# Performance work log

Measured on AMD Instinct MI355X. Metric: run time of the kernel, lower is better.

Reference implementation:

```python
import jax, jax.numpy as jnp
import numpy as np
from jax import lax

CONF_THRES = 0.5
IOU_THRES = 0.45
TOP_K = 2048  # fixed candidate cap for jit-friendly NMS


def _xywh2xyxy(x):
    # x: [N,4] center-x, center-y, w, h -> x1,y1,x2,y2
    xy, wh = x[:, :2], x[:, 2:4]
    return jnp.concatenate([xy - wh / 2, xy + wh / 2], axis=-1)


def _box_iou(b1, b2):
    # b1: [N,4], b2: [M,4] in xyxy -> [N,M]
    area1 = (b1[:, 2] - b1[:, 0]) * (b1[:, 3] - b1[:, 1])
    area2 = (b2[:, 2] - b2[:, 0]) * (b2[:, 3] - b2[:, 1])
    lt = jnp.maximum(b1[:, None, :2], b2[None, :, :2])
    rb = jnp.minimum(b1[:, None, 2:], b2[None, :, 2:])
    inter = jnp.clip(rb - lt, 0).prod(-1)
    return inter / (area1[:, None] + area2[None, :] - inter)


def _nms_per_image(x):
    # x: [N,16] = xywh(4), obj(1), landmarks(10), cls_score(1); nc=1 path
    obj = x[:, 4]
    conf = x[:, 15] * obj          # x[:,15:] *= x[:,4:5], then max over 1 class
    box = _xywh2xyxy(x[:, :4])
    valid = (obj > CONF_THRES) & (conf > CONF_THRES)
    score = jnp.where(valid, conf, -jnp.inf)

    topv, topi = lax.top_k(score, TOP_K)          # sorted descending
    valid_k = jnp.isfinite(topv)                  # [K]
    boxes_k = box[topi]                           # [K,4]; class offset c = 0 (nc=1)
    x_k = x[topi]                                 # [K,16]
    conf_k = conf[topi]

    iou = _box_iou(boxes_k, boxes_k)              # [K,K]

    def body(keep, inp):
        i, iou_row, v = inp
        suppressed = jnp.any(keep & (iou_row > IOU_THRES))
        keep_i = v & ~suppressed
        return keep.at[i].set(keep_i), keep_i

    keep, _ = lax.scan(body, jnp.zeros(TOP_K, bool),
                       (jnp.arange(TOP_K), iou, valid_k))

    # detection row: [x1,y1,x2,y2, conf, 10 landmarks, class(=0)]
    det = jnp.concatenate(
        [boxes_k, conf_k[:, None], x_k[:, 5:15],
         jnp.zeros((TOP_K, 1), x.dtype)], axis=1)
    return jnp.where(keep[:, None], det, jnp.zeros((), x.dtype))


def setup_inputs() -> dict:
    key = jax.random.key(0)
    prediction = jax.random.uniform(key, (8, 100800, 16), dtype=jnp.float32)
    return {"prediction": prediction}


def reference(prediction):
    # prediction: [B, N, 16] -> padded detections [B, TOP_K, 16]
    return jax.vmap(_nms_per_image)(prediction)
```

## Files before the change

kernel.cpp:

```cpp
#include <hip/hip_runtime.h>
#include <stdint.h>

#define NA    100800
#define NIMG  8
#define TOPK  2048
#define NBLK1 99
typedef unsigned long long u64;

__global__ __launch_bounds__(256) void k1_scan(const float* __restrict__ pred,
                                               unsigned* __restrict__ cand32,
                                               int* __restrict__ hist_blocks) {
    __shared__ int lhist[64];
    int t = threadIdx.x;
    int m = blockIdx.y;
    if (t < 64) lhist[t] = 0;
    __syncthreads();
    const float4* p4 = reinterpret_cast<const float4*>(pred + (size_t)m * NA * 16);
    int row0blk = blockIdx.x * 1024;
    for (int pass = 0; pass < 4; ++pass) {
        int row0 = row0blk + pass * 256;
        int i1 = row0 * 4 + 2 * t + 1;
        int i2 = i1 + 512;
        float4 A = make_float4(0.f, 0.f, 0.f, 0.f);
        float4 B = make_float4(0.f, 0.f, 0.f, 0.f);
        if ((i1 >> 2) < NA) A = p4[i1];
        if ((i2 >> 2) < NA) B = p4[i2];
        float aw = __shfl_xor(A.w, 1);
        float bw = __shfl_xor(B.w, 1);
        if (!(t & 1)) {
            int rA = row0 + (t >> 1);
            int rB = rA + 128;
            {
                float obj = A.x, x15 = aw;
                if (rA < NA) {
                    float conf = __fmul_rn(x15, obj);
                    unsigned cb = 0u;
                    if (obj > 0.5f && conf > 0.5f) {
                        cb = __float_as_uint(conf);
                        atomicAdd(&lhist[min(63, (int)((cb - 0x3F000000u) >> 17))], 1);
                    }
                    cand32[(size_t)m * NA + rA] = cb;
                }
            }
            {
                float obj = B.x, x15 = bw;
                if (rB < NA) {
                    float conf = __fmul_rn(x15, obj);
                    unsigned cb = 0u;
                    if (obj > 0.5f && conf > 0.5f) {
                        cb = __float_as_uint(conf);
                        atomicAdd(&lhist[min(63, (int)((cb - 0x3F000000u) >> 17))], 1);
                    }
                    cand32[(size_t)m * NA + rB] = cb;
                }
            }
        }
    }
    __syncthreads();
    if (t < 64) hist_blocks[((size_t)m * NBLK1 + blockIdx.x) * 64 + t] = lhist[t];
}

__global__ void k2a_cutoff(const int* __restrict__ hist_blocks, int* __restrict__ cut,
                           int* __restrict__ pos) {
    int m = blockIdx.x;
    int lane = threadIdx.x;
    int h = 0;
    #pragma unroll 4
    for (int b = 0; b < NBLK1; ++b)
        h += hist_blocks[((size_t)m * NBLK1 + b) * 64 + lane];
    #pragma unroll
    for (int off = 1; off < 64; off <<= 1) {
        int src = lane + off;
        int v = __shfl(h, src < 64 ? src : lane);
        h += (src < 64) ? v : 0;
    }
    int total  = __shfl(h, 0);
    int needed = min(total, TOPK);
    u64 bal = __ballot(h >= needed);
    int cutoff = 63 - __clzll(bal);
    if (lane == 0) { cut[m] = cutoff; pos[m] = 0; }
}

__global__ __launch_bounds__(1024) void k2b_compact(const unsigned* __restrict__ cand32,
                                                    const int* __restrict__ cut,
                                                    u64* __restrict__ comp,
                                                    int* __restrict__ pos) {
    __shared__ int wbase[16];
    __shared__ int sbase;
    int m = blockIdx.y;
    int i = blockIdx.x * 1024 + threadIdx.x;
    int lane = threadIdx.x & 63, wid = threadIdx.x >> 6;
    unsigned cb = (i < NA) ? cand32[(size_t)m * NA + i] : 0u;
    int c = cut[m];
    bool keep = false;
    if (cb) keep = min(63, (int)((cb - 0x3F000000u) >> 17)) >= c;
    u64 bal = __ballot(keep);
    int cnt = __popcll(bal);
    if (lane == 0) wbase[wid] = cnt;
    __syncthreads();
    if (threadIdx.x == 0) {
        int s = 0;
        #pragma unroll
        for (int w = 0; w < 16; ++w) { int v = wbase[w]; wbase[w] = s; s += v; }
        sbase = s ? atomicAdd(&pos[m], s) : 0;
    }
    __syncthreads();
    if (keep) {
        int p = sbase + wbase[wid] + (int)__popcll(bal & ((1ull << lane) - 1ull));
        if (p < 4096)
            comp[(size_t)m * 4096 + p] = ((u64)cb << 32) | (u64)(0xFFFFFFFFu - (unsigned)i);
    }
}

__global__ __launch_bounds__(1024) void k2c_rank(const u64* __restrict__ comp,
                                                 const int* __restrict__ pos,
                                                 const float* __restrict__ pred,
                                                 u64* __restrict__ sel,
                                                 float4* __restrict__ boxes) {
    __shared__ int fcnt[4096];
    __shared__ int fstart[4096];
    __shared__ u64 outb[4096];
    __shared__ int wsum[16];
    int m = blockIdx.x, t = threadIdx.x;
    int M = min(pos[m], 4096);
    const u64* c = comp + (size_t)m * 4096;
    #pragma unroll
    for (int r = 0; r < 4; ++r) { fcnt[t + r * 1024] = 0; outb[t + r * 1024] = 0ull; }
    __syncthreads();
    u64 kk[4]; int rb[4];
    #pragma unroll
    for (int r = 0; r < 4; ++r) {
        int i = t + r * 1024;
        kk[r] = 0ull; rb[r] = -1;
        if (i < M) {
            kk[r] = c[i];
            rb[r] = 4095 - (int)(((unsigned)(kk[r] >> 32) - 0x3F000000u) >> 11);
            atomicAdd(&fcnt[rb[r]], 1);
        }
    }
    __syncthreads();
    int c0 = fcnt[4 * t], c1 = fcnt[4 * t + 1], c2 = fcnt[4 * t + 2], c3 = fcnt[4 * t + 3];
    int s = c0 + c1 + c2 + c3;
    int lane = t & 63, w = t >> 6;
    int incl = s;
    #pragma unroll
    for (int off = 1; off < 64; off <<= 1) {
        int v = __shfl_up(incl, off);
        if (lane >= off) incl += v;
    }
    if (lane == 63) wsum[w] = incl;
    __syncthreads();
    if (w == 0) {
        int v = (lane < 16) ? wsum[lane] : 0;
        #pragma unroll
        for (int off = 1; off < 16; off <<= 1) {
            int u = __shfl_up(v, off);
            if (lane >= off) v += u;
        }
        if (lane < 16) wsum[lane] = v;
    }
    __syncthreads();
    int base = (w > 0 ? wsum[w - 1] : 0) + (incl - s);
    fstart[4 * t]     = base;
    fstart[4 * t + 1] = base + c0;
    fstart[4 * t + 2] = base + c0 + c1;
    fstart[4 * t + 3] = base + c0 + c1 + c2;
    __syncthreads();
    #pragma unroll
    for (int r = 0; r < 4; ++r) {
        if (rb[r] >= 0) {
            int old = atomicSub(&fcnt[rb[r]], 1);
            int slot = fstart[rb[r]] + old - 1;
            outb[slot] = kk[r];
        }
    }
    __syncthreads();
    #pragma unroll
    for (int r = 0; r < 4; ++r) {
        int b = t + r * 1024;
        int st = fstart[b];
        int en = (b < 4095) ? fstart[b + 1] : M;
        for (int x = st + 1; x < en; ++x) {
            u64 key = outb[x];
            int y = x - 1;
            while (y >= st && outb[y] < key) { outb[y + 1] = outb[y]; --y; }
            outb[y + 1] = key;
        }
    }
    __syncthreads();
    #pragma unroll
    for (int r = 0; r < 2; ++r) {
        int i = t + r * 1024;
        u64 key = outb[i];
        sel[(size_t)m * TOPK + i] = key;
        float4 b = make_float4(0.f, 0.f, 0.f, 0.f);
        if (key) {
            unsigned idx = 0xFFFFFFFFu - (unsigned)(key & 0xFFFFFFFFull);
            const float4* rv = reinterpret_cast<const float4*>(pred + ((size_t)m * NA + idx) * 16);
            float4 v = rv[0];
            float hw = __fmul_rn(v.z, 0.5f), hh = __fmul_rn(v.w, 0.5f);
            b.x = __fsub_rn(v.x, hw);
            b.y = __fsub_rn(v.y, hh);
            b.z = __fadd_rn(v.x, hw);
            b.w = __fadd_rn(v.y, hh);
        }
        boxes[(size_t)m * TOPK + i] = b;
    }
}

__global__ __launch_bounds__(1024) void k4_masks(const float4* __restrict__ boxes,
                                                 u64* __restrict__ maskT) {
    __shared__ float4 bx[TOPK];
    int m   = blockIdx.y;
    int grp = blockIdx.x;
    for (int i = threadIdx.x; i < TOPK; i += 1024)
        bx[i] = boxes[(size_t)m * TOPK + i];
    __syncthreads();

    int il = threadIdx.x & 31;
    int w  = threadIdx.x >> 5;
    int i  = grp * 32 + il;
    float4 b1 = bx[i];
    float a1 = __fmul_rn(__fsub_rn(b1.z, b1.x), __fsub_rn(b1.w, b1.y));
    u64 bits = 0ull;
    #pragma unroll 4
    for (int jj = 0; jj < 64; ++jj) {
        float4 b2 = bx[w * 64 + jj];
        float a2 = __fmul_rn(__fsub_rn(b2.z, b2.x), __fsub_rn(b2.w, b2.y));
        float iw = fmaxf(__fsub_rn(fminf(b1.z, b2.z), fmaxf(b1.x, b2.x)), 0.f);
        float ih = fmaxf(__fsub_rn(fminf(b1.w, b2.w), fmaxf(b1.y, b2.y)), 0.f);
        float inter = __fmul_rn(iw, ih);
        float uni   = __fsub_rn(__fadd_rn(a1, a2), inter);
        float iou   = __fdiv_rn(inter, uni);
        if (iou > 0.45f) bits |= (1ull << jj);
    }
    maskT[((size_t)m * 32 + w) * 2048 + i] = bits;
}

__global__ __launch_bounds__(1024) void k5_nms(const u64* __restrict__ sel,
                                               const u64* __restrict__ maskT,
                                               const float* __restrict__ pred,
                                               float4* __restrict__ out) {
    __shared__ u64 remv[32];
    __shared__ u64 kbshare[2];
    __shared__ u64 kws[32];
    int m = blockIdx.x;
    int t = threadIdx.x;
    int lane = t & 63;
    int wv = t >> 6;
    const u64* mt = maskT + (size_t)m * 32 * 2048;
    if (t < 32) remv[t] = 0ull;
    u64 dval = 0ull, sval = 0ull, tval = 0ull;
    u64 cfmask = 0ull;
    u64 mybit = 1ull << lane;
    u64 lowmask = mybit - 1ull;
    if (wv == 0) {
        dval = mt[(size_t)0 * 2048 + lane];
        sval = sel[(size_t)m * TOPK + lane];
        tval = mt[(size_t)0 * 2048 + 64 + lane];
    }
    __syncthreads();
    for (int blk = 0; blk < 32; ++blk) {
        if (wv == 0) {
            u64 dn = 0ull, sn = 0ull, tn = 0ull;
            if (blk < 31) {
                int r = (blk + 1) * 64 + lane;
                dn = mt[(size_t)(blk + 1) * 2048 + r];
                sn = sel[(size_t)m * TOPK + r];
                if (blk < 30) tn = mt[(size_t)(blk + 1) * 2048 + r + 64];
            }
            u64 ext = remv[blk];
            u64 validw = __ballot(sval != 0ull);
            u64 alive = validw & ~ext & ~cfmask;
            u64 kb = 0ull;
            while (alive) {
                u64 c = dval & alive & lowmask;
                u64 ready = __ballot(((alive & mybit) != 0ull) && (c == 0ull));
                kb |= ready;
                u64 removed = __ballot((dval & ready) != 0ull);
                alive &= ~(ready | removed);
            }
            cfmask = (blk < 31) ? __ballot((tval & kb) != 0ull) : 0ull;
            if (lane == 0) {
                kbshare[blk & 1] = kb;
                kws[blk] = kb;
            }
            dval = dn; sval = sn; tval = tn;
        } else if (blk >= 1) {
            u64 kb = kbshare[(blk - 1) & 1];
            int w1 = blk + wv;
            int w2 = blk + 15 + wv;
            u64 v1 = (w1 < 32) ? mt[(size_t)(blk - 1) * 2048 + w1 * 64 + lane] : 0ull;
            u64 v2 = (w2 < 32) ? mt[(size_t)(blk - 1) * 2048 + w2 * 64 + lane] : 0ull;
            u64 c1 = __ballot((v1 & kb) != 0ull);
            u64 c2 = __ballot((v2 & kb) != 0ull);
            if (w1 < 32 && lane == 0) remv[w1] |= c1;
            if (w2 < 32 && lane == 0) remv[w2] |= c2;
        }
        __syncthreads();
    }
    const u64* sl = sel + (size_t)m * TOPK;
    float4* om = out + (size_t)m * TOPK * 4;
    #pragma unroll
    for (int q = t; q < TOPK * 4; q += 1024) {
        int c4 = q & 3;
        int r  = q >> 2;
        float4 o = make_float4(0.f, 0.f, 0.f, 0.f);
        if ((kws[r >> 6] >> (r & 63)) & 1ull) {
            u64 key = sl[r];
            unsigned idx = 0xFFFFFFFFu - (unsigned)(key & 0xFFFFFFFFull);
            const float4* rv = reinterpret_cast<const float4*>(pred + ((size_t)m * NA + idx) * 16);
            float4 v = rv[c4];
            if (c4 == 0) {
                float hw = __fmul_rn(v.z, 0.5f), hh = __fmul_rn(v.w, 0.5f);
                o = make_float4(__fsub_rn(v.x, hw), __fsub_rn(v.y, hh),
                                __fadd_rn(v.x, hw), __fadd_rn(v.y, hh));
            } else if (c4 == 1) {
                o = make_float4(__uint_as_float((unsigned)(key >> 32)), v.y, v.z, v.w);
            } else if (c4 == 2) {
                o = v;
            } else {
                o = make_float4(v.x, v.y, v.z, 0.f);
            }
        }
        om[q] = o;
    }
}

extern "C" void kernel_launch(void* const* d_in, const int* in_sizes, int n_in,
                              void* d_out, int out_size, void* d_ws, size_t ws_size,
                              hipStream_t stream) {
    (void)in_sizes; (void)n_in; (void)out_size; (void)ws_size;
    const float* pred = (const float*)d_in[0];
    char* ws = (char*)d_ws;
    unsigned* cand32   = (unsigned*)(ws + 0);
    u64*      comp     = (u64*)     (ws + 3225600);
    u64*      sel      = (u64*)     (ws + 3487744);
    float4*   boxes    = (float4*)  (ws + 3618816);
    u64*      maskT    = (u64*)     (ws + 3880960);
    int*      histb    = (int*)     (ws + 8077312);
    int*      pos      = (int*)     (ws + 8280064);
    int*      cut      = (int*)     (ws + 8280096);
    float4*   out      = (float4*)d_out;

    hipLaunchKernelGGL(k1_scan,    dim3(NBLK1, NIMG),            dim3(256),  0, stream, pred, cand32, histb);
    hipLaunchKernelGGL(k2a_cutoff, dim3(NIMG),                   dim3(64),   0, stream, histb, cut, pos);
    hipLaunchKernelGGL(k2b_compact,dim3(NBLK1, NIMG),            dim3(1024), 0, stream, cand32, cut, comp, pos);
    hipLaunchKernelGGL(k2c_rank,   dim3(NIMG),                   dim3(1024), 0, stream, comp, pos, pred, sel, boxes);
    hipLaunchKernelGGL(k4_masks,   dim3(64, NIMG),               dim3(1024), 0, stream, boxes, maskT);
    hipLaunchKernelGGL(k5_nms,     dim3(NIMG),                   dim3(1024), 0, stream, sel, maskT, pred, out);
}
```

Before: 100.6 us.

## Fuse cutoff, compaction and ranking into one per-image kernel

Merges the histogram cutoff kernel, the grid-wide compaction kernel and the rank kernel into a single kernel with one 1024-thread block per image. Candidates are compacted straight into shared memory using per-wave atomics, so the global comp buffer and the pos and cut buffers go away along with two launches. In exchange, each image's full 100800-entry candidate array is now scanned by one block instead of being spread across 99 blocks, which lowers parallelism for that pass. It also makes the compaction order nondeterministic, though the later rank step sorts by key.

```diff
diff --git a/kernel.cpp b/kernel.cpp
--- a/kernel.cpp
+++ b/kernel.cpp
@@ -60,80 +60,73 @@
     if (t < 64) hist_blocks[((size_t)m * NBLK1 + blockIdx.x) * 64 + t] = lhist[t];
 }
 
-__global__ void k2a_cutoff(const int* __restrict__ hist_blocks, int* __restrict__ cut,
-                           int* __restrict__ pos) {
-    int m = blockIdx.x;
-    int lane = threadIdx.x;
-    int h = 0;
-    #pragma unroll 4
-    for (int b = 0; b < NBLK1; ++b)
-        h += hist_blocks[((size_t)m * NBLK1 + b) * 64 + lane];
-    #pragma unroll
-    for (int off = 1; off < 64; off <<= 1) {
-        int src = lane + off;
-        int v = __shfl(h, src < 64 ? src : lane);
-        h += (src < 64) ? v : 0;
-    }
-    int total  = __shfl(h, 0);
-    int needed = min(total, TOPK);
-    u64 bal = __ballot(h >= needed);
-    int cutoff = 63 - __clzll(bal);
-    if (lane == 0) { cut[m] = cutoff; pos[m] = 0; }
-}
-
-__global__ __launch_bounds__(1024) void k2b_compact(const unsigned* __restrict__ cand32,
-                                                    const int* __restrict__ cut,
-                                                    u64* __restrict__ comp,
-                                                    int* __restrict__ pos) {
-    __shared__ int wbase[16];
-    __shared__ int sbase;
-    int m = blockIdx.y;
-    int i = blockIdx.x * 1024 + threadIdx.x;
-    int lane = threadIdx.x & 63, wid = threadIdx.x >> 6;
-    unsigned cb = (i < NA) ? cand32[(size_t)m * NA + i] : 0u;
-    int c = cut[m];
-    bool keep = false;
-    if (cb) keep = min(63, (int)((cb - 0x3F000000u) >> 17)) >= c;
-    u64 bal = __ballot(keep);
-    int cnt = __popcll(bal);
-    if (lane == 0) wbase[wid] = cnt;
-    __syncthreads();
-    if (threadIdx.x == 0) {
-        int s = 0;
-        #pragma unroll
-        for (int w = 0; w < 16; ++w) { int v = wbase[w]; wbase[w] = s; s += v; }
-        sbase = s ? atomicAdd(&pos[m], s) : 0;
-    }
-    __syncthreads();
-    if (keep) {
-        int p = sbase + wbase[wid] + (int)__popcll(bal & ((1ull << lane) - 1ull));
-        if (p < 4096)
-            comp[(size_t)m * 4096 + p] = ((u64)cb << 32) | (u64)(0xFFFFFFFFu - (unsigned)i);
-    }
-}
-
-__global__ __launch_bounds__(1024) void k2c_rank(const u64* __restrict__ comp,
-                                                 const int* __restrict__ pos,
+__global__ __launch_bounds__(1024) void k2_fused(const unsigned* __restrict__ cand32,
+                                                 const int* __restrict__ hist_blocks,
                                                  const float* __restrict__ pred,
                                                  u64* __restrict__ sel,
                                                  float4* __restrict__ boxes) {
+    __shared__ int lhist[64];
     __shared__ int fcnt[4096];
     __shared__ int fstart[4096];
     __shared__ u64 outb[4096];
     __shared__ int wsum[16];
+    __shared__ int cutsh, msh;
     int m = blockIdx.x, t = threadIdx.x;
-    int M = min(pos[m], 4096);
-    const u64* c = comp + (size_t)m * 4096;
+    int lane = t & 63, w = t >> 6;
+    if (t < 64) lhist[t] = 0;
+    if (t == 0) msh = 0;
     #pragma unroll
     for (int r = 0; r < 4; ++r) { fcnt[t + r * 1024] = 0; outb[t + r * 1024] = 0ull; }
     __syncthreads();
+    {
+        int s = 0;
+        for (int b = w; b < NBLK1; b += 16)
+            s += hist_blocks[((size_t)m * NBLK1 + b) * 64 + lane];
+        if (s) atomicAdd(&lhist[lane], s);
+    }
+    __syncthreads();
+    if (w == 0) {
+        int h = lhist[lane];
+        #pragma unroll
+        for (int off = 1; off < 64; off <<= 1) {
+            int src = lane + off;
+            int v = __shfl(h, src < 64 ? src : lane);
+            h += (src < 64) ? v : 0;
+        }
+        int total  = __shfl(h, 0);
+        int needed = min(total, TOPK);
+        u64 bal = __ballot(h >= needed);
+        int cutoff = 63 - __clzll(bal);
+        if (lane == 0) cutsh = cutoff;
+    }
+    __syncthreads();
+    int cut = cutsh;
+    for (int i = t; i < NA; i += 1024) {
+        unsigned cb = cand32[(size_t)m * NA + i];
+        bool keep = false;
+        if (cb) keep = min(63, (int)((cb - 0x3F000000u) >> 17)) >= cut;
+        u64 bal = __ballot(keep);
+        if (bal) {
+            int cnt = __popcll(bal);
+            int base = 0;
+            if (lane == 0) base = atomicAdd(&msh, cnt);
+            base = __shfl(base, 0);
+            if (keep) {
+                int p = base + (int)__popcll(bal & ((1ull << lane) - 1ull));
+                if (p < 4096)
+                    outb[p] = ((u64)cb << 32) | (u64)(0xFFFFFFFFu - (unsigned)i);
+            }
+        }
+    }
+    __syncthreads();
+    int M = min(msh, 4096);
     u64 kk[4]; int rb[4];
     #pragma unroll
     for (int r = 0; r < 4; ++r) {
         int i = t + r * 1024;
         kk[r] = 0ull; rb[r] = -1;
         if (i < M) {
-            kk[r] = c[i];
+            kk[r] = outb[i];
             rb[r] = 4095 - (int)(((unsigned)(kk[r] >> 32) - 0x3F000000u) >> 11);
             atomicAdd(&fcnt[rb[r]], 1);
         }
@@ -141,7 +134,6 @@
     __syncthreads();
     int c0 = fcnt[4 * t], c1 = fcnt[4 * t + 1], c2 = fcnt[4 * t + 2], c3 = fcnt[4 * t + 3];
     int s = c0 + c1 + c2 + c3;
-    int lane = t & 63, w = t >> 6;
     int incl = s;
     #pragma unroll
     for (int off = 1; off < 64; off <<= 1) {
@@ -334,19 +326,14 @@
     const float* pred = (const float*)d_in[0];
     char* ws = (char*)d_ws;
     unsigned* cand32   = (unsigned*)(ws + 0);
-    u64*      comp     = (u64*)     (ws + 3225600);
-    u64*      sel      = (u64*)     (ws + 3487744);
-    float4*   boxes    = (float4*)  (ws + 3618816);
-    u64*      maskT    = (u64*)     (ws + 3880960);
-    int*      histb    = (int*)     (ws + 8077312);
-    int*      pos      = (int*)     (ws + 8280064);
-    int*      cut      = (int*)     (ws + 8280096);
+    u64*      sel      = (u64*)     (ws + 3225600);
+    float4*   boxes    = (float4*)  (ws + 3356672);
+    u64*      maskT    = (u64*)     (ws + 3618816);
+    int*      histb    = (int*)     (ws + 7813120);
     float4*   out      = (float4*)d_out;
 
-    hipLaunchKernelGGL(k1_scan,    dim3(NBLK1, NIMG),            dim3(256),  0, stream, pred, cand32, histb);
-    hipLaunchKernelGGL(k2a_cutoff, dim3(NIMG),                   dim3(64),   0, stream, histb, cut, pos);
-    hipLaunchKernelGGL(k2b_compact,dim3(NBLK1, NIMG),            dim3(1024), 0, stream, cand32, cut, comp, pos);
-    hipLaunchKernelGGL(k2c_rank,   dim3(NIMG),                   dim3(1024), 0, stream, comp, pos, pred, sel, boxes);
-    hipLaunchKernelGGL(k4_masks,   dim3(64, NIMG),               dim3(1024), 0, stream, boxes, maskT);
-    hipLaunchKernelGGL(k5_nms,     dim3(NIMG),                   dim3(1024), 0, stream, sel, maskT, pred, out);
-}
+    hipLaunchKernelGGL(k1_scan,   dim3(NBLK1, NIMG), dim3(256),  0, stream, pred, cand32, histb);
+    hipLaunchKernelGGL(k2_fused,  dim3(NIMG),        dim3(1024), 0, stream, cand32, histb, pred, sel, boxes);
+    hipLaunchKernelGGL(k4_masks,  dim3(64, NIMG),    dim3(1024), 0, stream, boxes, maskT);
+    hipLaunchKernelGGL(k5_nms,    dim3(NIMG),        dim3(1024), 0, stream, sel, maskT, pred, out);
+}
```

Result: slower. 125.1 us (+24.3%).
